# Optimization experiments

Hardware: AMD Instinct MI355X
Metric: run time of the kernel (lower is better)

## Reference

```python
import jax, jax.numpy as jnp
import numpy as np

N_NODES = 50000
N_EDGES = 800000
IN_DIM = 128
HIDDEN = 128
HEADS = 2
C = HIDDEN // HEADS  # per-head channels
N_CLASSES = 32
N_GRAPHS = 64
NEG_SLOPE = 0.2  # PyG GATConv default negative_slope


def setup_inputs() -> dict:
    key = jax.random.key(0)
    ks = jax.random.split(key, 16)
    x = jax.random.normal(ks[0], (N_NODES, IN_DIM), dtype=jnp.float32)
    edge_index = jax.random.randint(ks[1], (2, N_EDGES), 0, N_NODES, dtype=jnp.int64)
    batch = jnp.sort(jax.random.randint(ks[2], (N_NODES,), 0, N_GRAPHS, dtype=jnp.int64))
    s_in = 1.0 / np.sqrt(IN_DIM)
    s_h = 1.0 / np.sqrt(HIDDEN)
    s_c = 1.0 / np.sqrt(C)
    W1 = jax.random.normal(ks[3], (HEADS * C, IN_DIM), jnp.float32) * s_in
    att_src1 = jax.random.normal(ks[4], (HEADS, C), jnp.float32) * s_c
    att_dst1 = jax.random.normal(ks[5], (HEADS, C), jnp.float32) * s_c
    b1 = jnp.zeros((HEADS * C,), jnp.float32)
    W2 = jax.random.normal(ks[6], (HEADS * C, HIDDEN), jnp.float32) * s_h
    att_src2 = jax.random.normal(ks[7], (HEADS, C), jnp.float32) * s_c
    att_dst2 = jax.random.normal(ks[8], (HEADS, C), jnp.float32) * s_c
    b2 = jnp.zeros((HEADS * C,), jnp.float32)
    fc_w = jax.random.normal(ks[9], (N_CLASSES, HIDDEN), jnp.float32) * s_h
    fc_b = jnp.zeros((N_CLASSES,), jnp.float32)
    return {"x": x, "edge_index": edge_index, "batch": batch,
            "W1": W1, "att_src1": att_src1, "att_dst1": att_dst1, "b1": b1,
            "W2": W2, "att_src2": att_src2, "att_dst2": att_dst2, "b2": b2,
            "fc_w": fc_w, "fc_b": fc_b}


def gat_conv(x, edge_index, W, att_src, att_dst, bias):
    """PyG GATConv (concat=True, add_self_loops=True, negative_slope=0.2)."""
    N = x.shape[0]
    loops = jnp.arange(N, dtype=edge_index.dtype)
    src = jnp.concatenate([edge_index[0], loops])  # [E+N]
    dst = jnp.concatenate([edge_index[1], loops])
    xl = (x @ W.T).reshape(N, HEADS, C)  # [N,H,C]
    a_src = jnp.einsum('nhc,hc->nh', xl, att_src)  # [N,H]
    a_dst = jnp.einsum('nhc,hc->nh', xl, att_dst)
    alpha = jax.nn.leaky_relu(a_src[src] + a_dst[dst], NEG_SLOPE)  # [E+N,H]
    # segment softmax over incoming edges of each dst node
    amax = jax.ops.segment_max(alpha, dst, num_segments=N)
    amax = jnp.where(jnp.isfinite(amax), amax, 0.0)
    ex = jnp.exp(alpha - amax[dst])
    denom = jax.ops.segment_sum(ex, dst, num_segments=N)
    coeff = ex / jnp.maximum(denom[dst], 1e-16)  # [E+N,H]
    msg = xl[src] * coeff[:, :, None]  # [E+N,H,C]
    out = jax.ops.segment_sum(msg, dst, num_segments=N)  # [N,H,C]
    return out.reshape(N, HEADS * C) + bias


def reference(x, edge_index, batch, W1, att_src1, att_dst1, b1,
              W2, att_src2, att_dst2, b2, fc_w, fc_b):
    h = jax.nn.relu(gat_conv(x, edge_index, W1, att_src1, att_dst1, b1))
    h = jax.nn.relu(gat_conv(h, edge_index, W2, att_src2, att_dst2, b2))
    # global_mean_pool over graphs
    sums = jax.ops.segment_sum(h, batch, num_segments=N_GRAPHS)  # [G,HIDDEN]
    counts = jax.ops.segment_sum(jnp.ones((h.shape[0],), h.dtype), batch, num_segments=N_GRAPHS)
    pooled = sums / jnp.maximum(counts, 1.0)[:, None]
    return pooled @ fc_w.T + fc_b  # [G, N_CLASSES]
```

## Files before the change

### kernel.cpp

```cpp
#include <hip/hip_runtime.h>
#include <hip/hip_bf16.h>


#define NEG_SLOPE 0.2f

typedef short bf16x8 __attribute__((ext_vector_type(8)));
typedef float f32x4 __attribute__((ext_vector_type(4)));

__device__ __forceinline__ float lrelu(float x) { return x > 0.f ? x : NEG_SLOPE * x; }
__device__ __forceinline__ float bf2f(unsigned short u) { return __uint_as_float(((unsigned)u) << 16); }
__device__ __forceinline__ unsigned short f2bf(float f) {
    unsigned x = __float_as_uint(f);
    return (unsigned short)((x + 0x7fffu + ((x >> 16) & 1u)) >> 16);
}

__global__ __launch_bounds__(256) void wconv_hist(const float* __restrict__ W1, const float* __restrict__ W2,
                                                  unsigned short* __restrict__ Wb1, unsigned short* __restrict__ Wb2,
                                                  float* __restrict__ zbuf, int zn,
                                                  const int* __restrict__ ei, int* __restrict__ ph, int E) {
    __shared__ int hist[256];
    int t = threadIdx.x;
    int b = blockIdx.x;
    int i = b * 256 + t;
    if (i < 16384) Wb1[i] = f2bf(W1[i]);
    else if (i < 32768) Wb2[i - 16384] = f2bf(W2[i - 16384]);
    if (i < zn) zbuf[i] = 0.f;
    hist[t] = 0;
    __syncthreads();
    for (int e = i; e < E; e += 256 * 256)
        atomicAdd(&hist[ei[E + e] >> 8], 1);
    __syncthreads();
    ph[b * 256 + t] = hist[t];
}

__global__ __launch_bounds__(256) void bucket_scan(const int* __restrict__ ph, int* __restrict__ ebase,
                                                   int* __restrict__ bcur, int* __restrict__ offs,
                                                   int NB, int N, int E) {
    __shared__ int sc[256];
    int t = threadIdx.x;
    int cnt = 0;
    for (int b = 0; b < 256; ++b) cnt += ph[b * 256 + t];
    sc[t] = cnt;
    __syncthreads();
    for (int off = 1; off < 256; off <<= 1) {
        int x = (t >= off) ? sc[t - off] : 0;
        __syncthreads();
        sc[t] += x;
        __syncthreads();
    }
    int excl = sc[t] - cnt;
    if (t < NB) {
        ebase[t] = excl;
        bcur[t] = excl;
    }
    if (t == NB - 1) ebase[NB] = sc[t];
    if (t == 0) offs[N] = E + N;
}

__global__ __launch_bounds__(1024) void bucket_scatter(const int* __restrict__ ei, int* __restrict__ bcur,
                                                       unsigned* __restrict__ pk, int E) {
    __shared__ int hist[256];
    __shared__ int base[256];
    int t = threadIdx.x;
    if (t < 256) hist[t] = 0;
    __syncthreads();
    int eb = blockIdx.x * 16384;
    int d[16], s[16];
#pragma unroll
    for (int i = 0; i < 16; ++i) {
        int e = eb + i * 1024 + t;
        if (e < E) {
            d[i] = ei[E + e];
            s[i] = ei[e];
            atomicAdd(&hist[d[i] >> 8], 1);
        } else {
            d[i] = -1;
        }
    }
    __syncthreads();
    if (t < 256) {
        int c = hist[t];
        base[t] = c ? atomicAdd(&bcur[t], c) : 0;
        hist[t] = 0;
    }
    __syncthreads();
#pragma unroll
    for (int i = 0; i < 16; ++i) {
        if (d[i] >= 0) {
            int bk = d[i] >> 8;
            int r = atomicAdd(&hist[bk], 1);
            pk[base[bk] + r] = ((unsigned)s[i] << 8) | (unsigned)(d[i] & 255);
        }
    }
}

__global__ __launch_bounds__(256) void csr_build(const unsigned* __restrict__ pk, const int* __restrict__ ebase,
                                                 int* __restrict__ offs, int* __restrict__ ssrc, int N) {
    __shared__ int deg[256];
    __shared__ int curs[256];
    __shared__ int sc[256];
    int t = threadIdx.x;
    int b = blockIdx.x;
    deg[t] = 0;
    __syncthreads();
    int e0 = ebase[b], e1 = ebase[b + 1];
    for (int j = e0 + t; j < e1; j += 256) atomicAdd(&deg[pk[j] & 255], 1);
    __syncthreads();
    int nb0 = b * 256;
    int ncount = min(256, N - nb0);
    int v = (t < ncount) ? deg[t] + 1 : 0;
    sc[t] = v;
    __syncthreads();
    for (int off = 1; off < 256; off <<= 1) {
        int x = (t >= off) ? sc[t - off] : 0;
        __syncthreads();
        sc[t] += x;
        __syncthreads();
    }
    int nbase = e0 + b * 256;
    if (t < ncount) {
        int o = nbase + sc[t] - v;
        offs[nb0 + t] = o;
        ssrc[o] = nb0 + t;
        curs[t] = o + 1;
    }
    __syncthreads();
    for (int j = e0 + t; j < e1; j += 256) {
        unsigned e = pk[j];
        int pos = atomicAdd(&curs[e & 255], 1);
        ssrc[pos] = (int)(e >> 8);
    }
}

#define LDW 136
template <typename T>
__global__ __launch_bounds__(256) void gemm_kernel(const T* __restrict__ A, const unsigned short* __restrict__ Wb,
                                                   unsigned short* __restrict__ out,
                                                   const float* __restrict__ att_s, const float* __restrict__ att_d,
                                                   float* __restrict__ a_src, float* __restrict__ a_dst, int M) {
    __shared__ unsigned short Ws[128 * LDW];
    int tid = threadIdx.x;
    int m0 = blockIdx.x * 128;
#pragma unroll
    for (int i = 0; i < 8; ++i) {
        int slot = i * 256 + tid;
        int r = slot >> 4;
        int c8 = (slot & 15) << 3;
        *(uint4*)(&Ws[r * LDW + c8]) = *(const uint4*)(Wb + r * 128 + c8);
    }
    int w = tid >> 6, l = tid & 63;
    int lr = l & 15;
    int lk = (l >> 4) << 3;
    int row0 = m0 + w * 32 + lr;
    int row1 = row0 + 16;
    int r0c = min(row0, M - 1);
    int r1c = min(row1, M - 1);
    bf16x8 aA0, aA1, aA2, aA3, aB0, aB1, aB2, aB3;
    if constexpr (sizeof(T) == 4) {
        const float* Ar0 = (const float*)A + (size_t)r0c * 128 + lk;
        const float* Ar1 = (const float*)A + (size_t)r1c * 128 + lk;
#define ALOAD(dst, Ar, i) { float4 v0 = *(const float4*)((Ar) + (i) * 32); \
                            float4 v1 = *(const float4*)((Ar) + (i) * 32 + 4); \
                            dst = (bf16x8){(short)f2bf(v0.x), (short)f2bf(v0.y), (short)f2bf(v0.z), (short)f2bf(v0.w), \
                                           (short)f2bf(v1.x), (short)f2bf(v1.y), (short)f2bf(v1.z), (short)f2bf(v1.w)}; }
        ALOAD(aA0, Ar0, 0) ALOAD(aA1, Ar0, 1) ALOAD(aA2, Ar0, 2) ALOAD(aA3, Ar0, 3)
        ALOAD(aB0, Ar1, 0) ALOAD(aB1, Ar1, 1) ALOAD(aB2, Ar1, 2) ALOAD(aB3, Ar1, 3)
#undef ALOAD
    } else {
        const unsigned short* Ar0 = (const unsigned short*)A + (size_t)r0c * 128 + lk;
        const unsigned short* Ar1 = (const unsigned short*)A + (size_t)r1c * 128 + lk;
        aA0 = *(const bf16x8*)(Ar0 + 0);  aA1 = *(const bf16x8*)(Ar0 + 32);
        aA2 = *(const bf16x8*)(Ar0 + 64); aA3 = *(const bf16x8*)(Ar0 + 96);
        aB0 = *(const bf16x8*)(Ar1 + 0);  aB1 = *(const bf16x8*)(Ar1 + 32);
        aB2 = *(const bf16x8*)(Ar1 + 64); aB3 = *(const bf16x8*)(Ar1 + 96);
    }
    __syncthreads();
    f32x4 xA0 = {0.f, 0.f, 0.f, 0.f}, xA1 = xA0, xA2 = xA0, xA3 = xA0, xA4 = xA0, xA5 = xA0, xA6 = xA0, xA7 = xA0;
    f32x4 xB0 = xA0, xB1 = xA0, xB2 = xA0, xB3 = xA0, xB4 = xA0, xB5 = xA0, xB6 = xA0, xB7 = xA0;
#define MROW(ks, afA, afB)                                                                        \
    {                                                                                             \
        int kb = (ks) * 32 + lk;                                                                  \
        bf16x8 b0 = *(const bf16x8*)(&Ws[(0 * 16 + lr) * LDW + kb]);                              \
        bf16x8 b1 = *(const bf16x8*)(&Ws[(1 * 16 + lr) * LDW + kb]);                              \
        bf16x8 b2 = *(const bf16x8*)(&Ws[(2 * 16 + lr) * LDW + kb]);                              \
        bf16x8 b3 = *(const bf16x8*)(&Ws[(3 * 16 + lr) * LDW + kb]);                              \
        bf16x8 b4 = *(const bf16x8*)(&Ws[(4 * 16 + lr) * LDW + kb]);                              \
        bf16x8 b5 = *(const bf16x8*)(&Ws[(5 * 16 + lr) * LDW + kb]);                              \
        bf16x8 b6 = *(const bf16x8*)(&Ws[(6 * 16 + lr) * LDW + kb]);                              \
        bf16x8 b7 = *(const bf16x8*)(&Ws[(7 * 16 + lr) * LDW + kb]);                              \
        xA0 = __builtin_amdgcn_mfma_f32_16x16x32_bf16(afA, b0, xA0, 0, 0, 0);                     \
        xA1 = __builtin_amdgcn_mfma_f32_16x16x32_bf16(afA, b1, xA1, 0, 0, 0);                     \
        xA2 = __builtin_amdgcn_mfma_f32_16x16x32_bf16(afA, b2, xA2, 0, 0, 0);                     \
        xA3 = __builtin_amdgcn_mfma_f32_16x16x32_bf16(afA, b3, xA3, 0, 0, 0);                     \
        xA4 = __builtin_amdgcn_mfma_f32_16x16x32_bf16(afA, b4, xA4, 0, 0, 0);                     \
        xA5 = __builtin_amdgcn_mfma_f32_16x16x32_bf16(afA, b5, xA5, 0, 0, 0);                     \
        xA6 = __builtin_amdgcn_mfma_f32_16x16x32_bf16(afA, b6, xA6, 0, 0, 0);                     \
        xA7 = __builtin_amdgcn_mfma_f32_16x16x32_bf16(afA, b7, xA7, 0, 0, 0);                     \
        xB0 = __builtin_amdgcn_mfma_f32_16x16x32_bf16(afB, b0, xB0, 0, 0, 0);                     \
        xB1 = __builtin_amdgcn_mfma_f32_16x16x32_bf16(afB, b1, xB1, 0, 0, 0);                     \
        xB2 = __builtin_amdgcn_mfma_f32_16x16x32_bf16(afB, b2, xB2, 0, 0, 0);                     \
        xB3 = __builtin_amdgcn_mfma_f32_16x16x32_bf16(afB, b3, xB3, 0, 0, 0);                     \
        xB4 = __builtin_amdgcn_mfma_f32_16x16x32_bf16(afB, b4, xB4, 0, 0, 0);                     \
        xB5 = __builtin_amdgcn_mfma_f32_16x16x32_bf16(afB, b5, xB5, 0, 0, 0);                     \
        xB6 = __builtin_amdgcn_mfma_f32_16x16x32_bf16(afB, b6, xB6, 0, 0, 0);                     \
        xB7 = __builtin_amdgcn_mfma_f32_16x16x32_bf16(afB, b7, xB7, 0, 0, 0);                     \
    }
    MROW(0, aA0, aB0) MROW(1, aA1, aB1) MROW(2, aA2, aB2) MROW(3, aA3, aB3)
#undef MROW
    float as0 = att_s[lr], as1 = att_s[16 + lr], as2 = att_s[32 + lr], as3 = att_s[48 + lr];
    float as4 = att_s[64 + lr], as5 = att_s[80 + lr], as6 = att_s[96 + lr], as7 = att_s[112 + lr];
    float ad0 = att_d[lr], ad1 = att_d[16 + lr], ad2 = att_d[32 + lr], ad3 = att_d[48 + lr];
    float ad4 = att_d[64 + lr], ad5 = att_d[80 + lr], ad6 = att_d[96 + lr], ad7 = att_d[112 + lr];
#define EPILOG(x0, x1, x2, x3, x4, x5, x6, x7, rb)                                                \
    {                                                                                             \
        int rbase = (rb);                                                                         \
        _Pragma("unroll")                                                                         \
        for (int j = 0; j < 4; ++j) {                                                             \
            int m = rbase + j;                                                                    \
            if (m < M) {                                                                          \
                unsigned ob = (unsigned)m * 128 + (unsigned)lr;                                   \
                out[ob + 0] = f2bf(x0[j]);   out[ob + 16] = f2bf(x1[j]);                          \
                out[ob + 32] = f2bf(x2[j]);  out[ob + 48] = f2bf(x3[j]);                          \
                out[ob + 64] = f2bf(x4[j]);  out[ob + 80] = f2bf(x5[j]);                          \
                out[ob + 96] = f2bf(x6[j]);  out[ob + 112] = f2bf(x7[j]);                         \
            }                                                                                     \
        }                                                                                         \
        _Pragma("unroll")                                                                         \
        for (int j = 0; j < 4; ++j) {                                                             \
            float ps0 = x0[j] * as0 + x1[j] * as1 + x2[j] * as2 + x3[j] * as3;                    \
            float pd0 = x0[j] * ad0 + x1[j] * ad1 + x2[j] * ad2 + x3[j] * ad3;                    \
            float ps1 = x4[j] * as4 + x5[j] * as5 + x6[j] * as6 + x7[j] * as7;                    \
            float pd1 = x4[j] * ad4 + x5[j] * ad5 + x6[j] * ad6 + x7[j] * ad7;                    \
            _Pragma("unroll")                                                                     \
            for (int off = 1; off < 16; off <<= 1) {                                              \
                ps0 += __shfl_xor(ps0, off);                                                      \
                pd0 += __shfl_xor(pd0, off);                                                      \
                ps1 += __shfl_xor(ps1, off);                                                      \
                pd1 += __shfl_xor(pd1, off);                                                      \
            }                                                                                     \
            if (lr == 0) {                                                                        \
                int m = rbase + j;                                                                \
                if (m < M) {                                                                      \
                    a_src[m * 2 + 0] = ps0;                                                       \
                    a_dst[m * 2 + 0] = pd0;                                                       \
                    a_src[m * 2 + 1] = ps1;                                                       \
                    a_dst[m * 2 + 1] = pd1;                                                       \
                }                                                                                 \
            }                                                                                     \
        }                                                                                         \
    }
    EPILOG(xA0, xA1, xA2, xA3, xA4, xA5, xA6, xA7, m0 + w * 32 + ((l >> 4) << 2))
    EPILOG(xB0, xB1, xB2, xB3, xB4, xB5, xB6, xB7, m0 + w * 32 + 16 + ((l >> 4) << 2))
#undef EPILOG
}

#define MAXD 128
__global__ __launch_bounds__(256) void gat_node_kernel(const unsigned short* __restrict__ XLb,
                                                       const float* __restrict__ a_src, const float* __restrict__ a_dst,
                                                       const int* __restrict__ offs, const int* __restrict__ ssrc,
                                                       const float* __restrict__ bias,
                                                       unsigned short* __restrict__ out, int N) {
    __shared__ float coeff[4][2][MAXD];
    __shared__ int srcs[4][MAXD];
    int t = threadIdx.x;
    int w = t >> 6, l = t & 63;
    int n = blockIdx.x * 4 + w;
    if (n >= N) return;
    int h = l >> 5, sl = l & 31;
    int c = 2 * l;
    int j0 = offs[n], j1 = offs[n + 1];
    int deg = j1 - j0;
    float ad = a_dst[n * 2 + h];
    float acc0 = 0.f, acc1 = 0.f;
    if (deg <= MAXD) {
        float m = -1e30f;
        for (int k = sl; k < deg; k += 32) {
            int s = ssrc[j0 + k];
            if (h == 0) srcs[w][k] = s;
            float al = lrelu(a_src[s * 2 + h] + ad);
            coeff[w][h][k] = al;
            m = fmaxf(m, al);
        }
#pragma unroll
        for (int off = 16; off > 0; off >>= 1) m = fmaxf(m, __shfl_xor(m, off));
        float sum = 0.f;
        for (int k = sl; k < deg; k += 32) {
            float e = __expf(coeff[w][h][k] - m);
            coeff[w][h][k] = e;
            sum += e;
        }
#pragma unroll
        for (int off = 16; off > 0; off >>= 1) sum += __shfl_xor(sum, off);
        float inv = 1.f / fmaxf(sum, 1e-16f);
        int j = 0;
        for (; j + 7 < deg; j += 8) {
            float c0 = coeff[w][h][j + 0], c1 = coeff[w][h][j + 1];
            float c2 = coeff[w][h][j + 2], c3 = coeff[w][h][j + 3];
            float c4 = coeff[w][h][j + 4], c5 = coeff[w][h][j + 5];
            float c6 = coeff[w][h][j + 6], c7 = coeff[w][h][j + 7];
            unsigned s0 = (unsigned)srcs[w][j + 0], s1 = (unsigned)srcs[w][j + 1];
            unsigned s2 = (unsigned)srcs[w][j + 2], s3 = (unsigned)srcs[w][j + 3];
            unsigned s4 = (unsigned)srcs[w][j + 4], s5 = (unsigned)srcs[w][j + 5];
            unsigned s6 = (unsigned)srcs[w][j + 6], s7 = (unsigned)srcs[w][j + 7];
            unsigned u0 = *(const unsigned*)(XLb + (s0 << 7) + c);
            unsigned u1 = *(const unsigned*)(XLb + (s1 << 7) + c);
            unsigned u2 = *(const unsigned*)(XLb + (s2 << 7) + c);
            unsigned u3 = *(const unsigned*)(XLb + (s3 << 7) + c);
            unsigned u4 = *(const unsigned*)(XLb + (s4 << 7) + c);
            unsigned u5 = *(const unsigned*)(XLb + (s5 << 7) + c);
            unsigned u6 = *(const unsigned*)(XLb + (s6 << 7) + c);
            unsigned u7 = *(const unsigned*)(XLb + (s7 << 7) + c);
            acc0 += c0 * __uint_as_float(u0 << 16) + c1 * __uint_as_float(u1 << 16)
                  + c2 * __uint_as_float(u2 << 16) + c3 * __uint_as_float(u3 << 16)
                  + c4 * __uint_as_float(u4 << 16) + c5 * __uint_as_float(u5 << 16)
                  + c6 * __uint_as_float(u6 << 16) + c7 * __uint_as_float(u7 << 16);
            acc1 += c0 * __uint_as_float(u0 & 0xffff0000u) + c1 * __uint_as_float(u1 & 0xffff0000u)
                  + c2 * __uint_as_float(u2 & 0xffff0000u) + c3 * __uint_as_float(u3 & 0xffff0000u)
                  + c4 * __uint_as_float(u4 & 0xffff0000u) + c5 * __uint_as_float(u5 & 0xffff0000u)
                  + c6 * __uint_as_float(u6 & 0xffff0000u) + c7 * __uint_as_float(u7 & 0xffff0000u);
        }
        for (; j + 3 < deg; j += 4) {
            float c0 = coeff[w][h][j + 0], c1 = coeff[w][h][j + 1];
            float c2 = coeff[w][h][j + 2], c3 = coeff[w][h][j + 3];
            unsigned s0 = (unsigned)srcs[w][j + 0], s1 = (unsigned)srcs[w][j + 1];
            unsigned s2 = (unsigned)srcs[w][j + 2], s3 = (unsigned)srcs[w][j + 3];
            unsigned u0 = *(const unsigned*)(XLb + (s0 << 7) + c);
            unsigned u1 = *(const unsigned*)(XLb + (s1 << 7) + c);
            unsigned u2 = *(const unsigned*)(XLb + (s2 << 7) + c);
            unsigned u3 = *(const unsigned*)(XLb + (s3 << 7) + c);
            acc0 += c0 * __uint_as_float(u0 << 16) + c1 * __uint_as_float(u1 << 16)
                  + c2 * __uint_as_float(u2 << 16) + c3 * __uint_as_float(u3 << 16);
            acc1 += c0 * __uint_as_float(u0 & 0xffff0000u) + c1 * __uint_as_float(u1 & 0xffff0000u)
                  + c2 * __uint_as_float(u2 & 0xffff0000u) + c3 * __uint_as_float(u3 & 0xffff0000u);
        }
        for (; j < deg; ++j) {
            float c0 = coeff[w][h][j];
            unsigned s0 = (unsigned)srcs[w][j];
            unsigned u0 = *(const unsigned*)(XLb + (s0 << 7) + c);
            acc0 += c0 * __uint_as_float(u0 << 16);
            acc1 += c0 * __uint_as_float(u0 & 0xffff0000u);
        }
        acc0 *= inv;
        acc1 *= inv;
    } else {
        float m = -1e30f;
        for (int k = sl; k < deg; k += 32) {
            int s = ssrc[j0 + k];
            m = fmaxf(m, lrelu(a_src[s * 2 + h] + ad));
        }
#pragma unroll
        for (int off = 16; off > 0; off >>= 1) m = fmaxf(m, __shfl_xor(m, off));
        float sum = 0.f;
        for (int k = sl; k < deg; k += 32) {
            int s = ssrc[j0 + k];
            sum += __expf(lrelu(a_src[s * 2 + h] + ad) - m);
        }
#pragma unroll
        for (int off = 16; off > 0; off >>= 1) sum += __shfl_xor(sum, off);
        float inv = 1.f / fmaxf(sum, 1e-16f);
        for (int j = 0; j < deg; ++j) {
            unsigned s = (unsigned)ssrc[j0 + j];
            float cc = __expf(lrelu(a_src[s * 2 + h] + ad) - m) * inv;
            unsigned u0 = *(const unsigned*)(XLb + (s << 7) + c);
            acc0 += cc * __uint_as_float(u0 << 16);
            acc1 += cc * __uint_as_float(u0 & 0xffff0000u);
        }
    }
    float o0 = fmaxf(acc0 + bias[c], 0.f);
    float o1 = fmaxf(acc1 + bias[c + 1], 0.f);
    *(unsigned*)(out + ((unsigned)n << 7) + c) = (unsigned)f2bf(o0) | ((unsigned)f2bf(o1) << 16);
}

#define PB 128
__global__ __launch_bounds__(128) void pool_kernel(const unsigned short* __restrict__ Hb,
                                                   const int* __restrict__ batch,
                                                   float* __restrict__ pooled, int* __restrict__ counts, int N) {
    __shared__ unsigned short Hs[PB * 128];
    __shared__ int bs[PB];
    int t = threadIdx.x;
    int base = blockIdx.x * PB;
    int lim = min(PB, N - base);
#pragma unroll
    for (int i = 0; i < 16; ++i) {
        int slot = i * 128 + t;
        int r = slot >> 4;
        int c8 = (slot & 15) << 3;
        uint4 u = make_uint4(0, 0, 0, 0);
        int n0 = base + r;
        if (n0 < N) u = *(const uint4*)(Hb + (size_t)n0 * 128 + c8);
        *(uint4*)(&Hs[r * 128 + c8]) = u;
    }
    if (t < lim) bs[t] = batch[base + t];
    __syncthreads();
    float acc = 0.f;
    int cur = bs[0];
    int runstart = 0;
    for (int i = 0; i < lim; ++i) {
        int g = bs[i];
        if (g != cur) {
            atomicAdd(&pooled[cur * 128 + t], acc);
            if (t == 0) atomicAdd(&counts[cur], i - runstart);
            cur = g;
            acc = 0.f;
            runstart = i;
        }
        acc += bf2f(Hs[i * 128 + t]);
    }
    atomicAdd(&pooled[cur * 128 + t], acc);
    if (t == 0) atomicAdd(&counts[cur], lim - runstart);
}

__global__ void final_kernel(const float* __restrict__ pooled, const int* __restrict__ counts,
                             const float* __restrict__ fc_w, const float* __restrict__ fc_b,
                             float* __restrict__ out) {
    int idx = blockIdx.x * 256 + threadIdx.x;
    if (idx >= 64 * 32) return;
    int g = idx >> 5, k = idx & 31;
    float invc = 1.f / fmaxf((float)counts[g], 1.f);
    float s = 0.f;
#pragma unroll 4
    for (int c = 0; c < 128; ++c) s += pooled[g * 128 + c] * fc_w[k * 128 + c];
    out[idx] = s * invc + fc_b[k];
}

extern "C" void kernel_launch(void* const* d_in, const int* in_sizes, int n_in,
                              void* d_out, int out_size, void* d_ws, size_t ws_size,
                              hipStream_t stream) {
    const float* x = (const float*)d_in[0];
    const int* ei = (const int*)d_in[1];
    const int* batch = (const int*)d_in[2];
    const float* W1 = (const float*)d_in[3];
    const float* as1 = (const float*)d_in[4];
    const float* ad1 = (const float*)d_in[5];
    const float* b1 = (const float*)d_in[6];
    const float* W2 = (const float*)d_in[7];
    const float* as2 = (const float*)d_in[8];
    const float* ad2 = (const float*)d_in[9];
    const float* b2 = (const float*)d_in[10];
    const float* fcw = (const float*)d_in[11];
    const float* fcb = (const float*)d_in[12];
    float* out = (float*)d_out;

    const int N = in_sizes[0] / 128;
    const int E = in_sizes[1] / 2;
    const int EN = E + N;
    const int NB = (N + 255) >> 8;

    char* p = (char*)d_ws;
    auto alloc = [&](size_t bytes) -> char* {
        char* r = p;
        p += (bytes + 255) & ~(size_t)255;
        return r;
    };
    unsigned short* XLb = (unsigned short*)alloc((size_t)N * 128 * 2);
    unsigned short* Hb = (unsigned short*)alloc((size_t)N * 128 * 2);
    float* a_src = (float*)alloc((size_t)N * 2 * 4);
    float* a_dst = (float*)alloc((size_t)N * 2 * 4);
    int* offs = (int*)alloc((size_t)(N + 1) * 4);
    int* ssrc = (int*)alloc((size_t)EN * 4);
    unsigned* pk = (unsigned*)alloc((size_t)E * 4);
    int* ebase = (int*)alloc((size_t)(NB + 1) * 4);
    int* bcur = (int*)alloc((size_t)NB * 4);
    int* ph = (int*)alloc(256 * 256 * 4);
    unsigned short* Wb1 = (unsigned short*)alloc(16384 * 2);
    unsigned short* Wb2 = (unsigned short*)alloc(16384 * 2);
    float* pooled = (float*)alloc((8192 + 64) * 4);
    int* counts = (int*)(pooled + 8192);
    int zn = 8192 + 64;

    const int TB = 256;
    int gGemm = (N + 127) / 128;
    int gWave = (N + 3) / 4;

    wconv_hist<<<256, TB, 0, stream>>>(W1, W2, Wb1, Wb2, pooled, zn, ei, ph, E);
    bucket_scan<<<1, TB, 0, stream>>>(ph, ebase, bcur, offs, NB, N, E);
    bucket_scatter<<<(E + 16383) / 16384, 1024, 0, stream>>>(ei, bcur, pk, E);
    csr_build<<<NB, TB, 0, stream>>>(pk, ebase, offs, ssrc, N);

    gemm_kernel<float><<<gGemm, TB, 0, stream>>>(x, Wb1, XLb, as1, ad1, a_src, a_dst, N);
    gat_node_kernel<<<gWave, TB, 0, stream>>>(XLb, a_src, a_dst, offs, ssrc, b1, Hb, N);

    gemm_kernel<unsigned short><<<gGemm, TB, 0, stream>>>(Hb, Wb2, XLb, as2, ad2, a_src, a_dst, N);
    gat_node_kernel<<<gWave, TB, 0, stream>>>(XLb, a_src, a_dst, offs, ssrc, b2, Hb, N);

    pool_kernel<<<(N + PB - 1) / PB, 128, 0, stream>>>(Hb, batch, pooled, counts, N);
    final_kernel<<<8, TB, 0, stream>>>(pooled, counts, fcw, fcb, out);
}
```

Measured before the change: 249.4 us.

## Replace histogram and scan passes with fixed-capacity edge buckets and prefetch gathers

Result: faster. 234.1 us (-6.2%).

```diff
diff --git a/kernel.cpp b/kernel.cpp
--- a/kernel.cpp
+++ b/kernel.cpp
@@ -3,6 +3,7 @@
 
 
 #define NEG_SLOPE 0.2f
+#define CAP 6144
 
 typedef short bf16x8 __attribute__((ext_vector_type(8)));
 typedef float f32x4 __attribute__((ext_vector_type(4)));
@@ -14,47 +15,13 @@
     return (unsigned short)((x + 0x7fffu + ((x >> 16) & 1u)) >> 16);
 }
 
-__global__ __launch_bounds__(256) void wconv_hist(const float* __restrict__ W1, const float* __restrict__ W2,
-                                                  unsigned short* __restrict__ Wb1, unsigned short* __restrict__ Wb2,
-                                                  float* __restrict__ zbuf, int zn,
-                                                  const int* __restrict__ ei, int* __restrict__ ph, int E) {
-    __shared__ int hist[256];
-    int t = threadIdx.x;
-    int b = blockIdx.x;
-    int i = b * 256 + t;
+__global__ __launch_bounds__(256) void wconv(const float* __restrict__ W1, const float* __restrict__ W2,
+                                             unsigned short* __restrict__ Wb1, unsigned short* __restrict__ Wb2,
+                                             float* __restrict__ zbuf, int zn) {
+    int i = blockIdx.x * 256 + threadIdx.x;
     if (i < 16384) Wb1[i] = f2bf(W1[i]);
     else if (i < 32768) Wb2[i - 16384] = f2bf(W2[i - 16384]);
     if (i < zn) zbuf[i] = 0.f;
-    hist[t] = 0;
-    __syncthreads();
-    for (int e = i; e < E; e += 256 * 256)
-        atomicAdd(&hist[ei[E + e] >> 8], 1);
-    __syncthreads();
-    ph[b * 256 + t] = hist[t];
-}
-
-__global__ __launch_bounds__(256) void bucket_scan(const int* __restrict__ ph, int* __restrict__ ebase,
-                                                   int* __restrict__ bcur, int* __restrict__ offs,
-                                                   int NB, int N, int E) {
-    __shared__ int sc[256];
-    int t = threadIdx.x;
-    int cnt = 0;
-    for (int b = 0; b < 256; ++b) cnt += ph[b * 256 + t];
-    sc[t] = cnt;
-    __syncthreads();
-    for (int off = 1; off < 256; off <<= 1) {
-        int x = (t >= off) ? sc[t - off] : 0;
-        __syncthreads();
-        sc[t] += x;
-        __syncthreads();
-    }
-    int excl = sc[t] - cnt;
-    if (t < NB) {
-        ebase[t] = excl;
-        bcur[t] = excl;
-    }
-    if (t == NB - 1) ebase[NB] = sc[t];
-    if (t == 0) offs[N] = E + N;
 }
 
 __global__ __launch_bounds__(1024) void bucket_scatter(const int* __restrict__ ei, int* __restrict__ bcur,
@@ -89,27 +56,24 @@
         if (d[i] >= 0) {
             int bk = d[i] >> 8;
             int r = atomicAdd(&hist[bk], 1);
-            pk[base[bk] + r] = ((unsigned)s[i] << 8) | (unsigned)(d[i] & 255);
-        }
-    }
-}
-
-__global__ __launch_bounds__(256) void csr_build(const unsigned* __restrict__ pk, const int* __restrict__ ebase,
-                                                 int* __restrict__ offs, int* __restrict__ ssrc, int N) {
+            int slot = base[bk] + r;
+            if (slot < CAP) pk[bk * CAP + slot] = ((unsigned)s[i] << 8) | (unsigned)(d[i] & 255);
+        }
+    }
+}
+
+__global__ __launch_bounds__(256) void csr_build(const unsigned* __restrict__ pk, const int* __restrict__ bcnt,
+                                                 int* __restrict__ offs, int* __restrict__ ssrc,
+                                                 int N, int E, int NB) {
     __shared__ int deg[256];
     __shared__ int curs[256];
     __shared__ int sc[256];
+    __shared__ int e0_s, cnt_s;
     int t = threadIdx.x;
     int b = blockIdx.x;
+    int cnt = (t < NB) ? bcnt[t] : 0;
+    sc[t] = cnt;
     deg[t] = 0;
-    __syncthreads();
-    int e0 = ebase[b], e1 = ebase[b + 1];
-    for (int j = e0 + t; j < e1; j += 256) atomicAdd(&deg[pk[j] & 255], 1);
-    __syncthreads();
-    int nb0 = b * 256;
-    int ncount = min(256, N - nb0);
-    int v = (t < ncount) ? deg[t] + 1 : 0;
-    sc[t] = v;
     __syncthreads();
     for (int off = 1; off < 256; off <<= 1) {
         int x = (t >= off) ? sc[t - off] : 0;
@@ -117,16 +81,38 @@
         sc[t] += x;
         __syncthreads();
     }
-    int nbase = e0 + b * 256;
+    if (t == b) {
+        e0_s = sc[t] - cnt;
+        cnt_s = min(cnt, CAP);
+    }
+    __syncthreads();
+    int e0 = e0_s;
+    int mycnt = cnt_s;
+    const unsigned* mypk = pk + (size_t)b * CAP;
+    for (int j = t; j < mycnt; j += 256) atomicAdd(&deg[mypk[j] & 255], 1);
+    __syncthreads();
+    int nb0 = b * 256;
+    int ncount = min(256, N - nb0);
+    int v = (t < ncount) ? deg[t] + 1 : 0;
+    sc[t] = v;
+    __syncthreads();
+    for (int off = 1; off < 256; off <<= 1) {
+        int x = (t >= off) ? sc[t - off] : 0;
+        __syncthreads();
+        sc[t] += x;
+        __syncthreads();
+    }
+    int nbase = e0 + nb0;
     if (t < ncount) {
         int o = nbase + sc[t] - v;
         offs[nb0 + t] = o;
         ssrc[o] = nb0 + t;
         curs[t] = o + 1;
     }
-    __syncthreads();
-    for (int j = e0 + t; j < e1; j += 256) {
-        unsigned e = pk[j];
+    if (b == NB - 1 && t == 0) offs[N] = E + N;
+    __syncthreads();
+    for (int j = t; j < mycnt; j += 256) {
+        unsigned e = mypk[j];
         int pos = atomicAdd(&curs[e & 255], 1);
         ssrc[pos] = (int)(e >> 8);
     }
@@ -281,6 +267,18 @@
             coeff[w][h][k] = al;
             m = fmaxf(m, al);
         }
+        unsigned pu0 = 0, pu1 = 0, pu2 = 0, pu3 = 0, pu4 = 0, pu5 = 0, pu6 = 0, pu7 = 0;
+        bool pf = (deg >= 8);
+        if (pf) {
+            pu0 = *(const unsigned*)(XLb + ((unsigned)srcs[w][0] << 7) + c);
+            pu1 = *(const unsigned*)(XLb + ((unsigned)srcs[w][1] << 7) + c);
+            pu2 = *(const unsigned*)(XLb + ((unsigned)srcs[w][2] << 7) + c);
+            pu3 = *(const unsigned*)(XLb + ((unsigned)srcs[w][3] << 7) + c);
+            pu4 = *(const unsigned*)(XLb + ((unsigned)srcs[w][4] << 7) + c);
+            pu5 = *(const unsigned*)(XLb + ((unsigned)srcs[w][5] << 7) + c);
+            pu6 = *(const unsigned*)(XLb + ((unsigned)srcs[w][6] << 7) + c);
+            pu7 = *(const unsigned*)(XLb + ((unsigned)srcs[w][7] << 7) + c);
+        }
 #pragma unroll
         for (int off = 16; off > 0; off >>= 1) m = fmaxf(m, __shfl_xor(m, off));
         float sum = 0.f;
@@ -293,6 +291,19 @@
         for (int off = 16; off > 0; off >>= 1) sum += __shfl_xor(sum, off);
         float inv = 1.f / fmaxf(sum, 1e-16f);
         int j = 0;
+        if (pf) {
+            float c0 = coeff[w][h][0], c1 = coeff[w][h][1], c2 = coeff[w][h][2], c3 = coeff[w][h][3];
+            float c4 = coeff[w][h][4], c5 = coeff[w][h][5], c6 = coeff[w][h][6], c7 = coeff[w][h][7];
+            acc0 += c0 * __uint_as_float(pu0 << 16) + c1 * __uint_as_float(pu1 << 16)
+                  + c2 * __uint_as_float(pu2 << 16) + c3 * __uint_as_float(pu3 << 16)
+                  + c4 * __uint_as_float(pu4 << 16) + c5 * __uint_as_float(pu5 << 16)
+                  + c6 * __uint_as_float(pu6 << 16) + c7 * __uint_as_float(pu7 << 16);
+            acc1 += c0 * __uint_as_float(pu0 & 0xffff0000u) + c1 * __uint_as_float(pu1 & 0xffff0000u)
+                  + c2 * __uint_as_float(pu2 & 0xffff0000u) + c3 * __uint_as_float(pu3 & 0xffff0000u)
+                  + c4 * __uint_as_float(pu4 & 0xffff0000u) + c5 * __uint_as_float(pu5 & 0xffff0000u)
+                  + c6 * __uint_as_float(pu6 & 0xffff0000u) + c7 * __uint_as_float(pu7 & 0xffff0000u);
+            j = 8;
+        }
         for (; j + 7 < deg; j += 8) {
             float c0 = coeff[w][h][j + 0], c1 = coeff[w][h][j + 1];
             float c2 = coeff[w][h][j + 2], c3 = coeff[w][h][j + 3];
@@ -458,24 +469,21 @@
     float* a_dst = (float*)alloc((size_t)N * 2 * 4);
     int* offs = (int*)alloc((size_t)(N + 1) * 4);
     int* ssrc = (int*)alloc((size_t)EN * 4);
-    unsigned* pk = (unsigned*)alloc((size_t)E * 4);
-    int* ebase = (int*)alloc((size_t)(NB + 1) * 4);
-    int* bcur = (int*)alloc((size_t)NB * 4);
-    int* ph = (int*)alloc(256 * 256 * 4);
+    unsigned* pk = (unsigned*)alloc((size_t)NB * CAP * 4);
     unsigned short* Wb1 = (unsigned short*)alloc(16384 * 2);
     unsigned short* Wb2 = (unsigned short*)alloc(16384 * 2);
-    float* pooled = (float*)alloc((8192 + 64) * 4);
+    float* pooled = (float*)alloc((8192 + 64 + 256) * 4);
     int* counts = (int*)(pooled + 8192);
-    int zn = 8192 + 64;
+    int* bcur = (int*)(pooled + 8192 + 64);
+    int zn = 8192 + 64 + 256;
 
     const int TB = 256;
     int gGemm = (N + 127) / 128;
     int gWave = (N + 3) / 4;
 
-    wconv_hist<<<256, TB, 0, stream>>>(W1, W2, Wb1, Wb2, pooled, zn, ei, ph, E);
-    bucket_scan<<<1, TB, 0, stream>>>(ph, ebase, bcur, offs, NB, N, E);
+    wconv<<<128, TB, 0, stream>>>(W1, W2, Wb1, Wb2, pooled, zn);
     bucket_scatter<<<(E + 16383) / 16384, 1024, 0, stream>>>(ei, bcur, pk, E);
-    csr_build<<<NB, TB, 0, stream>>>(pk, ebase, offs, ssrc, N);
+    csr_build<<<NB, TB, 0, stream>>>(pk, bcur, offs, ssrc, N, E, NB);
 
     gemm_kernel<float><<<gGemm, TB, 0, stream>>>(x, Wb1, XLb, as1, ad1, a_src, a_dst, N);
     gat_node_kernel<<<gWave, TB, 0, stream>>>(XLb, a_src, a_dst, offs, ssrc, b1, Hb, N);
```
